# Kernel optimization log

Hardware: AMD Instinct MI355X
Metric: run time of the kernel (lower is better)

## Reference

```python
import jax, jax.numpy as jnp
import numpy as np

NUM_HEADS = 32
NUM_KV_HEADS = 8  # num_heads // 4 (GQA)
HEAD_DIM = 64     # hidden_size // num_heads
ROPE_BASE = 10000.0


def _rotate_half(x):
    x1, x2 = jnp.split(x, 2, axis=-1)
    return jnp.concatenate((-x2, x1), axis=-1)


def _rope_cos_sin(seq_len, dtype):
    inv_freq = 1.0 / (ROPE_BASE ** (jnp.arange(0, HEAD_DIM, 2, dtype=jnp.float32) / HEAD_DIM))
    t = jnp.arange(seq_len, dtype=jnp.float32)
    freqs = jnp.outer(t, inv_freq)                 # [S, HEAD_DIM//2]
    emb = jnp.concatenate((freqs, freqs), axis=-1) # [S, HEAD_DIM]
    return jnp.cos(emb).astype(dtype), jnp.sin(emb).astype(dtype)


def setup_inputs() -> dict:
    key = jax.random.key(0)
    ks = jax.random.split(key, 5)
    B, S, H = 1, 2048, 2048
    KV = NUM_KV_HEADS * HEAD_DIM  # 512
    s = 0.02
    return {
        "hidden_states": jax.random.normal(ks[0], (B, S, H), jnp.float32),
        "Wq": jax.random.normal(ks[1], (H, H), jnp.float32) * s,
        "Wk": jax.random.normal(ks[2], (KV, H), jnp.float32) * s,
        "Wv": jax.random.normal(ks[3], (KV, H), jnp.float32) * s,
        "Wo": jax.random.normal(ks[4], (H, H), jnp.float32) * s,
    }


def reference(hidden_states, Wq, Wk, Wv, Wo):
    B, S, H = hidden_states.shape
    dtype = hidden_states.dtype
    # QKV projections (nn.Linear with weight [out,in], no bias)
    q = jnp.einsum("bsh,oh->bso", hidden_states, Wq)
    k = jnp.einsum("bsh,oh->bso", hidden_states, Wk)
    v = jnp.einsum("bsh,oh->bso", hidden_states, Wv)
    q = q.reshape(B, S, NUM_HEADS, HEAD_DIM).transpose(0, 2, 1, 3)      # [B,H,S,D]
    k = k.reshape(B, S, NUM_KV_HEADS, HEAD_DIM).transpose(0, 2, 1, 3)   # [B,KV,S,D]
    v = v.reshape(B, S, NUM_KV_HEADS, HEAD_DIM).transpose(0, 2, 1, 3)
    # RoPE
    cos, sin = _rope_cos_sin(S, dtype)  # [S,D] broadcast over batch/heads
    q = q * cos + _rotate_half(q) * sin
    k = k * cos + _rotate_half(k) * sin
    # GQA: repeat_interleave KV heads
    groups = NUM_HEADS // NUM_KV_HEADS
    k = jnp.repeat(k, groups, axis=1)
    v = jnp.repeat(v, groups, axis=1)
    # Attention: scores in fp32 softmax, causal mask (additive)
    scale = 1.0 / np.sqrt(HEAD_DIM)
    scores = jnp.einsum("bhqd,bhkd->bhqk", q, k) * scale
    causal = jnp.tril(jnp.ones((S, S), dtype=bool))
    scores = jnp.where(causal, scores, jnp.finfo(jnp.float32).min)
    probs = jax.nn.softmax(scores.astype(jnp.float32), axis=-1).astype(dtype)
    attn = jnp.einsum("bhqk,bhkd->bhqd", probs, v)
    attn = attn.transpose(0, 2, 1, 3).reshape(B, S, H)
    return jnp.einsum("bsh,oh->bso", attn, Wo)
```

## Files before the change

### kernel.cpp

```cpp
#include <hip/hip_runtime.h>
#include <hip/hip_bf16.h>
#include <math.h>

typedef __hip_bfloat16 bf16;
typedef __attribute__((ext_vector_type(8))) short short8;
typedef __attribute__((ext_vector_type(4))) short short4v;
typedef __attribute__((ext_vector_type(4))) float floatx4;

#define MFMA16(a, b, c) __builtin_amdgcn_mfma_f32_16x16x32_bf16((a), (b), (c), 0, 0, 0)

typedef const __attribute__((address_space(1))) void* as1_cvp;
typedef __attribute__((address_space(3))) void* as3_vp;

__device__ __forceinline__ void gload_lds16(const bf16* g, bf16* lds_uni) {
    __builtin_amdgcn_global_load_lds((as1_cvp)g, (as3_vp)lds_uni, 16, 0, 0);
}

__global__ __launch_bounds__(256) void cvt_all(
    const float* __restrict__ a0, const float* __restrict__ a1,
    const float* __restrict__ a2, const float* __restrict__ a3,
    const float* __restrict__ a4,
    bf16* __restrict__ d0, bf16* __restrict__ d1, bf16* __restrict__ d2,
    bf16* __restrict__ d3, bf16* __restrict__ d4)
{
    const int b = blockIdx.x;
    const float* src; bf16* dst; int off;
    if (b < 2048)      { src = a0; dst = d0; off = b; }
    else if (b < 4096) { src = a1; dst = d1; off = b - 2048; }
    else if (b < 4608) { src = a2; dst = d2; off = b - 4096; }
    else if (b < 5120) { src = a3; dst = d3; off = b - 4608; }
    else               { src = a4; dst = d4; off = b - 5120; }
    const int i = (off * 256 + threadIdx.x) * 8;
    const float4 x = *(const float4*)(src + i);
    const float4 y = *(const float4*)(src + i + 4);
    bf16 t[8];
    t[0] = __float2bfloat16(x.x); t[1] = __float2bfloat16(x.y);
    t[2] = __float2bfloat16(x.z); t[3] = __float2bfloat16(x.w);
    t[4] = __float2bfloat16(y.x); t[5] = __float2bfloat16(y.y);
    t[6] = __float2bfloat16(y.z); t[7] = __float2bfloat16(y.w);
    *(short8*)(dst + i) = *(const short8*)t;
}

__global__ __launch_bounds__(256) void gemm_qkv(
    const bf16* __restrict__ A, const bf16* __restrict__ Wq,
    const bf16* __restrict__ Wk, const bf16* __restrict__ Wv,
    bf16* __restrict__ qb, bf16* __restrict__ kb, bf16* __restrict__ vt)
{
    constexpr int K = 2048;
    __shared__ bf16 As[128 * 32];
    __shared__ bf16 Bs[128 * 32];

    const int tid  = threadIdx.x;
    const int lane = tid & 63;
    const int w    = tid >> 6;
    const int wm   = w >> 1, wn = w & 1;
    const int quad = lane >> 4, l15 = lane & 15;
    const int bx = blockIdx.x, by = blockIdx.y;

    const bf16* Bp; int bxl, mode;
    if (bx < 16)      { Bp = Wq; bxl = bx;      mode = 0; }
    else if (bx < 20) { Bp = Wk; bxl = bx - 16; mode = 1; }
    else              { Bp = Wv; bxl = bx - 20; mode = 2; }

    floatx4 acc[4][4];
#pragma unroll
    for (int i = 0; i < 4; ++i)
#pragma unroll
        for (int j = 0; j < 4; ++j) {
            floatx4 z = {0.f, 0.f, 0.f, 0.f};
            acc[i][j] = z;
        }

    const int srow = tid >> 2;
    const int sch  = (tid & 3) * 8;
    const bf16* gA = A  + (size_t)(by * 128 + srow) * K + sch;
    const bf16* gB = Bp + (size_t)(bxl * 128 + srow) * K + sch;
    const size_t K64 = (size_t)64 * K;
    bf16* ldsA0 = As + w * 512;
    bf16* ldsA1 = As + 2048 + w * 512;
    bf16* ldsB0 = Bs + w * 512;
    bf16* ldsB1 = Bs + 2048 + w * 512;

    for (int k0 = 0; k0 < K; k0 += 32) {
        gload_lds16(gA + k0,        ldsA0);
        gload_lds16(gA + K64 + k0,  ldsA1);
        gload_lds16(gB + k0,        ldsB0);
        gload_lds16(gB + K64 + k0,  ldsB1);
        __syncthreads();

        short8 af[4], bfrag[4];
#pragma unroll
        for (int i = 0; i < 4; ++i)
            af[i] = *(const short8*)&As[(wm * 64 + i * 16 + l15) * 32 + quad * 8];
#pragma unroll
        for (int j = 0; j < 4; ++j)
            bfrag[j] = *(const short8*)&Bs[(wn * 64 + j * 16 + l15) * 32 + quad * 8];
#pragma unroll
        for (int i = 0; i < 4; ++i)
#pragma unroll
            for (int j = 0; j < 4; ++j)
                acc[i][j] = MFMA16(af[i], bfrag[j], acc[i][j]);
        __syncthreads();
    }

    if (mode == 2) {
#pragma unroll
        for (int i = 0; i < 4; ++i)
#pragma unroll
            for (int j = 0; j < 4; ++j) {
                const int col = bxl * 128 + wn * 64 + j * 16 + l15;
                const int rowb = by * 128 + wm * 64 + i * 16 + quad * 4;
                bf16 t[4];
#pragma unroll
                for (int r = 0; r < 4; ++r) t[r] = __float2bfloat16(acc[i][j][r]);
                *(short4v*)&vt[(size_t)col * 2048 + rowb] = *(const short4v*)t;
            }
    } else {
        const int Nn = (mode == 0) ? 2048 : 512;
        bf16* C = (mode == 0) ? qb : kb;
        const float scale = (mode == 0) ? 0.125f : 1.0f;
        const float LOG2_1E4 = 13.28771237954945f;
        const float ifr0 = exp2f(-((float)l15) * (LOG2_1E4 / 32.f));
        const float ifr1 = exp2f(-((float)(16 + l15)) * (LOG2_1E4 / 32.f));
#pragma unroll
        for (int i = 0; i < 4; ++i) {
#pragma unroll
            for (int r = 0; r < 4; ++r) {
                const int row = by * 128 + wm * 64 + i * 16 + quad * 4 + r;
                float s0, c0, s1, c1;
                sincosf((float)row * ifr0, &s0, &c0);
                sincosf((float)row * ifr1, &s1, &c1);
#pragma unroll
                for (int j = 0; j < 4; ++j) {
                    const float x  = acc[i][j][r];
                    const float xp = acc[i][j ^ 2][r];
                    const float cs = (j & 1) ? c1 : c0;
                    const float sn = (j & 1) ? s1 : s0;
                    const float oo = (x * cs + ((j < 2) ? -xp : xp) * sn) * scale;
                    const int col = bxl * 128 + wn * 64 + j * 16 + l15;
                    C[(size_t)row * Nn + col] = __float2bfloat16(oo);
                }
            }
        }
    }
}

__global__ __launch_bounds__(256) void gemm_out(
    const bf16* __restrict__ A, const bf16* __restrict__ B, float* __restrict__ C,
    int N, int K)
{
    __shared__ bf16 As[128 * 32];
    __shared__ bf16 Bs[128 * 32];

    const int tid  = threadIdx.x;
    const int lane = tid & 63;
    const int w    = tid >> 6;
    const int wm   = w >> 1, wn = w & 1;
    const int quad = lane >> 4, l15 = lane & 15;
    const int bx = blockIdx.x, by = blockIdx.y;

    floatx4 acc[4][4];
#pragma unroll
    for (int i = 0; i < 4; ++i)
#pragma unroll
        for (int j = 0; j < 4; ++j) {
            floatx4 z = {0.f, 0.f, 0.f, 0.f};
            acc[i][j] = z;
        }

    const int srow = tid >> 2;
    const int sch  = (tid & 3) * 8;
    const bf16* gA = A + (size_t)(by * 128 + srow) * K + sch;
    const bf16* gB = B + (size_t)(bx * 128 + srow) * K + sch;
    const size_t K64 = (size_t)64 * K;
    bf16* ldsA0 = As + w * 512;
    bf16* ldsA1 = As + 2048 + w * 512;
    bf16* ldsB0 = Bs + w * 512;
    bf16* ldsB1 = Bs + 2048 + w * 512;

    for (int k0 = 0; k0 < K; k0 += 32) {
        gload_lds16(gA + k0,        ldsA0);
        gload_lds16(gA + K64 + k0,  ldsA1);
        gload_lds16(gB + k0,        ldsB0);
        gload_lds16(gB + K64 + k0,  ldsB1);
        __syncthreads();

        short8 af[4], bfrag[4];
#pragma unroll
        for (int i = 0; i < 4; ++i)
            af[i] = *(const short8*)&As[(wm * 64 + i * 16 + l15) * 32 + quad * 8];
#pragma unroll
        for (int j = 0; j < 4; ++j)
            bfrag[j] = *(const short8*)&Bs[(wn * 64 + j * 16 + l15) * 32 + quad * 8];
#pragma unroll
        for (int i = 0; i < 4; ++i)
#pragma unroll
            for (int j = 0; j < 4; ++j)
                acc[i][j] = MFMA16(af[i], bfrag[j], acc[i][j]);
        __syncthreads();
    }

#pragma unroll
    for (int i = 0; i < 4; ++i)
#pragma unroll
        for (int j = 0; j < 4; ++j)
#pragma unroll
            for (int r = 0; r < 4; ++r) {
                const int row = by * 128 + wm * 64 + i * 16 + quad * 4 + r;
                const int col = bx * 128 + wn * 64 + j * 16 + l15;
                C[(size_t)row * N + col] = acc[i][j][r];
            }
}

__global__ __launch_bounds__(256) void fattn4(
    const bf16* __restrict__ q, const bf16* __restrict__ k,
    const bf16* __restrict__ vt, bf16* __restrict__ o)
{
    __shared__ bf16 Ks[2][64 * 72];
    __shared__ bf16 Vs[2][64 * 72];
    __shared__ bf16 Ps[4][16 * 68];

    const int tpair = blockIdx.x;
    const int h = blockIdx.y;
    const int kvh = h >> 2;
    const int tid = threadIdx.x, lane = tid & 63, w = tid >> 6;
    const int quad = lane >> 4, l15 = lane & 15;
    bf16* P = Ps[w];

    short ob[8];
#pragma unroll
    for (int e = 0; e < 8; ++e) ob[e] = (short)0x3F80;
    const short8 ones = *(const short8*)ob;

    const int srow = tid >> 3;
    const int ch8  = (tid & 7) * 8;
    const bf16* kg = k  + (size_t)kvh * 64 + ch8;
    const bf16* vg = vt + (size_t)(kvh * 64 + srow) * 2048 + ch8;

#pragma unroll 1
    for (int ph = 0; ph < 2; ++ph) {
        const int a = ph ? (31 - tpair) : tpair;
        const int qrow0 = a * 64 + w * 16;

        short8 qf[2];
#pragma unroll
        for (int ks = 0; ks < 2; ++ks)
            qf[ks] = *(const short8*)&q[(size_t)(qrow0 + l15) * 2048 + h * 64 + ks * 32 + quad * 8];

        floatx4 o_acc[4], l_acc;
#pragma unroll
        for (int n4 = 0; n4 < 4; ++n4) {
            floatx4 z = {0.f, 0.f, 0.f, 0.f};
            o_acc[n4] = z;
        }
        { floatx4 z = {0.f, 0.f, 0.f, 0.f}; l_acc = z; }

        {
            short8 k0 = *(const short8*)(kg + (size_t)srow * 512);
            short8 k1 = *(const short8*)(kg + (size_t)(srow + 32) * 512);
            short8 v0 = *(const short8*)(vg);
            short8 v1 = *(const short8*)(vg + (size_t)32 * 2048);
            *(short8*)&Ks[0][srow * 72 + ch8]        = k0;
            *(short8*)&Ks[0][(srow + 32) * 72 + ch8] = k1;
            *(short8*)&Vs[0][srow * 72 + ch8]        = v0;
            *(short8*)&Vs[0][(srow + 32) * 72 + ch8] = v1;
        }
        __syncthreads();

        for (int kt = 0; kt <= a; ++kt) {
            const int buf = kt & 1;

            short8 nk0, nk1, nv0, nv1;
            if (kt < a) {
                const size_t kr = (size_t)((kt + 1) * 64) * 512;
                nk0 = *(const short8*)(kg + kr + (size_t)srow * 512);
                nk1 = *(const short8*)(kg + kr + (size_t)(srow + 32) * 512);
                nv0 = *(const short8*)(vg + (kt + 1) * 64);
                nv1 = *(const short8*)(vg + (size_t)32 * 2048 + (kt + 1) * 64);
            }

            floatx4 s_acc[4];
#pragma unroll
            for (int n = 0; n < 4; ++n) {
                floatx4 z = {0.f, 0.f, 0.f, 0.f};
                s_acc[n] = z;
            }
#pragma unroll
            for (int n = 0; n < 4; ++n)
#pragma unroll
                for (int ks = 0; ks < 2; ++ks) {
                    const short8 kf = *(const short8*)&Ks[buf][(n * 16 + l15) * 72 + ks * 32 + quad * 8];
                    s_acc[n] = MFMA16(qf[ks], kf, s_acc[n]);
                }

            if (kt < a) {
#pragma unroll
                for (int n = 0; n < 4; ++n)
#pragma unroll
                    for (int r = 0; r < 4; ++r)
                        P[(quad * 4 + r) * 68 + n * 16 + l15] = __float2bfloat16(__expf(s_acc[n][r]));
            } else {
#pragma unroll
                for (int n = 0; n < 4; ++n)
#pragma unroll
                    for (int r = 0; r < 4; ++r) {
                        const bool ok = (n * 16 + l15) <= (w * 16 + quad * 4 + r);
                        const float p = ok ? __expf(s_acc[n][r]) : 0.f;
                        P[(quad * 4 + r) * 68 + n * 16 + l15] = __float2bfloat16(p);
                    }
            }

#pragma unroll
            for (int ks2 = 0; ks2 < 2; ++ks2) {
                const short8 pf = *(const short8*)&P[l15 * 68 + ks2 * 32 + quad * 8];
                l_acc = MFMA16(pf, ones, l_acc);
#pragma unroll
                for (int n4 = 0; n4 < 4; ++n4) {
                    const short8 vf = *(const short8*)&Vs[buf][(n4 * 16 + l15) * 72 + ks2 * 32 + quad * 8];
                    o_acc[n4] = MFMA16(pf, vf, o_acc[n4]);
                }
            }

            if (kt < a) {
                *(short8*)&Ks[buf ^ 1][srow * 72 + ch8]        = nk0;
                *(short8*)&Ks[buf ^ 1][(srow + 32) * 72 + ch8] = nk1;
                *(short8*)&Vs[buf ^ 1][srow * 72 + ch8]        = nv0;
                *(short8*)&Vs[buf ^ 1][(srow + 32) * 72 + ch8] = nv1;
            }
            __syncthreads();
        }

#pragma unroll
        for (int n4 = 0; n4 < 4; ++n4)
#pragma unroll
            for (int r = 0; r < 4; ++r) {
                const float val = o_acc[n4][r] / l_acc[r];
                const int row = qrow0 + quad * 4 + r;
                const int col = h * 64 + n4 * 16 + l15;
                o[(size_t)row * 2048 + col] = __float2bfloat16(val);
            }
    }
}

extern "C" void kernel_launch(void* const* d_in, const int* in_sizes, int n_in,
                              void* d_out, int out_size, void* d_ws, size_t ws_size,
                              hipStream_t stream)
{
    const float* hs = (const float*)d_in[0];
    const float* Wq = (const float*)d_in[1];
    const float* Wk = (const float*)d_in[2];
    const float* Wv = (const float*)d_in[3];
    const float* Wo = (const float*)d_in[4];
    float* out = (float*)d_out;

    bf16* ws  = (bf16*)d_ws;
    bf16* hsb = ws;
    bf16* Wqb = hsb + 4194304;
    bf16* Wkb = Wqb + 4194304;
    bf16* Wvb = Wkb + 1048576;
    bf16* Wob = Wvb + 1048576;
    bf16* qb  = Wob + 4194304;
    bf16* kb  = qb  + 4194304;
    bf16* vtb = kb  + 1048576;
    bf16* ab  = vtb + 1048576;

    dim3 blk(256);
    cvt_all<<<7168, blk, 0, stream>>>(hs, Wq, Wk, Wv, Wo, hsb, Wqb, Wkb, Wvb, Wob);
    gemm_qkv<<<dim3(24, 16), blk, 0, stream>>>(hsb, Wqb, Wkb, Wvb, qb, kb, vtb);
    fattn4<<<dim3(16, 32), blk, 0, stream>>>(qb, kb, vtb, ab);
    gemm_out<<<dim3(16, 16), blk, 0, stream>>>(ab, Wob, out, 2048, 2048);
}
```

Measured before the change: 248.9 us.

## Use 128x64 GEMM tiles with K=64 steps and transpose attention score MFMA

Both projection GEMMs now use 128x64 block tiles with four warps each owning 32 rows, and load 64 K-elements per barrier pair. This doubles the grid size so more CUs are occupied, and halves the number of sync iterations. In exchange, each block reuses the A tile across fewer output columns. The attention kernel swaps the MFMA operands for QK^T so each lane holds four consecutive keys, which allows vectorized 4-element P stores into LDS instead of scalar stores.

```diff
diff --git a/kernel.cpp b/kernel.cpp
--- a/kernel.cpp
+++ b/kernel.cpp
@@ -41,30 +41,56 @@
     *(short8*)(dst + i) = *(const short8*)t;
 }
 
+#define GEMM_K_LOOP_12864(KB)                                                   \
+    for (int k0 = 0; k0 < (KB); k0 += 64) {                                     \
+        gload_lds16(gA + k0,            ldsA);                                  \
+        gload_lds16(gA + A64 + k0,      ldsA + 2048);                           \
+        gload_lds16(gB + k0,            ldsB);                                  \
+        gload_lds16(gA + k0 + 32,       ldsA + 4096);                           \
+        gload_lds16(gA + A64 + k0 + 32, ldsA + 6144);                           \
+        gload_lds16(gB + k0 + 32,       ldsB + 2048);                           \
+        __syncthreads();                                                        \
+        _Pragma("unroll")                                                       \
+        for (int hh = 0; hh < 2; ++hh) {                                        \
+            short8 af[2], bfr[4];                                               \
+            _Pragma("unroll")                                                   \
+            for (int i = 0; i < 2; ++i)                                         \
+                af[i] = *(const short8*)&As[hh * 4096 + (w * 32 + i * 16 + l15) * 32 + quad * 8]; \
+            _Pragma("unroll")                                                   \
+            for (int j = 0; j < 4; ++j)                                         \
+                bfr[j] = *(const short8*)&Bs[hh * 2048 + (j * 16 + l15) * 32 + quad * 8]; \
+            _Pragma("unroll")                                                   \
+            for (int i = 0; i < 2; ++i)                                         \
+                _Pragma("unroll")                                               \
+                for (int j = 0; j < 4; ++j)                                     \
+                    acc[i][j] = MFMA16(af[i], bfr[j], acc[i][j]);               \
+        }                                                                       \
+        __syncthreads();                                                        \
+    }
+
 __global__ __launch_bounds__(256) void gemm_qkv(
     const bf16* __restrict__ A, const bf16* __restrict__ Wq,
     const bf16* __restrict__ Wk, const bf16* __restrict__ Wv,
     bf16* __restrict__ qb, bf16* __restrict__ kb, bf16* __restrict__ vt)
 {
-    constexpr int K = 2048;
-    __shared__ bf16 As[128 * 32];
-    __shared__ bf16 Bs[128 * 32];
+    constexpr int LDK = 2048;
+    __shared__ bf16 As[2 * 128 * 32];
+    __shared__ bf16 Bs[2 * 64 * 32];
 
     const int tid  = threadIdx.x;
     const int lane = tid & 63;
     const int w    = tid >> 6;
-    const int wm   = w >> 1, wn = w & 1;
     const int quad = lane >> 4, l15 = lane & 15;
     const int bx = blockIdx.x, by = blockIdx.y;
 
     const bf16* Bp; int bxl, mode;
-    if (bx < 16)      { Bp = Wq; bxl = bx;      mode = 0; }
-    else if (bx < 20) { Bp = Wk; bxl = bx - 16; mode = 1; }
-    else              { Bp = Wv; bxl = bx - 20; mode = 2; }
-
-    floatx4 acc[4][4];
-#pragma unroll
-    for (int i = 0; i < 4; ++i)
+    if (bx < 32)      { Bp = Wq; bxl = bx;      mode = 0; }
+    else if (bx < 40) { Bp = Wk; bxl = bx - 32; mode = 1; }
+    else              { Bp = Wv; bxl = bx - 40; mode = 2; }
+
+    floatx4 acc[2][4];
+#pragma unroll
+    for (int i = 0; i < 2; ++i)
 #pragma unroll
         for (int j = 0; j < 4; ++j) {
             floatx4 z = {0.f, 0.f, 0.f, 0.f};
@@ -73,60 +99,38 @@
 
     const int srow = tid >> 2;
     const int sch  = (tid & 3) * 8;
-    const bf16* gA = A  + (size_t)(by * 128 + srow) * K + sch;
-    const bf16* gB = Bp + (size_t)(bxl * 128 + srow) * K + sch;
-    const size_t K64 = (size_t)64 * K;
-    bf16* ldsA0 = As + w * 512;
-    bf16* ldsA1 = As + 2048 + w * 512;
-    bf16* ldsB0 = Bs + w * 512;
-    bf16* ldsB1 = Bs + 2048 + w * 512;
-
-    for (int k0 = 0; k0 < K; k0 += 32) {
-        gload_lds16(gA + k0,        ldsA0);
-        gload_lds16(gA + K64 + k0,  ldsA1);
-        gload_lds16(gB + k0,        ldsB0);
-        gload_lds16(gB + K64 + k0,  ldsB1);
-        __syncthreads();
-
-        short8 af[4], bfrag[4];
-#pragma unroll
-        for (int i = 0; i < 4; ++i)
-            af[i] = *(const short8*)&As[(wm * 64 + i * 16 + l15) * 32 + quad * 8];
-#pragma unroll
-        for (int j = 0; j < 4; ++j)
-            bfrag[j] = *(const short8*)&Bs[(wn * 64 + j * 16 + l15) * 32 + quad * 8];
-#pragma unroll
-        for (int i = 0; i < 4; ++i)
-#pragma unroll
-            for (int j = 0; j < 4; ++j)
-                acc[i][j] = MFMA16(af[i], bfrag[j], acc[i][j]);
-        __syncthreads();
-    }
+    const bf16* gA = A  + (size_t)(by * 128 + srow) * LDK + sch;
+    const bf16* gB = Bp + (size_t)(bxl * 64 + srow) * LDK + sch;
+    const size_t A64 = (size_t)64 * LDK;
+    bf16* ldsA = As + w * 512;
+    bf16* ldsB = Bs + w * 512;
+
+    GEMM_K_LOOP_12864(LDK)
 
     if (mode == 2) {
 #pragma unroll
-        for (int i = 0; i < 4; ++i)
+        for (int i = 0; i < 2; ++i)
 #pragma unroll
             for (int j = 0; j < 4; ++j) {
-                const int col = bxl * 128 + wn * 64 + j * 16 + l15;
-                const int rowb = by * 128 + wm * 64 + i * 16 + quad * 4;
+                const int col = bxl * 64 + j * 16 + l15;
+                const int rowb = by * 128 + w * 32 + i * 16 + quad * 4;
                 bf16 t[4];
 #pragma unroll
                 for (int r = 0; r < 4; ++r) t[r] = __float2bfloat16(acc[i][j][r]);
                 *(short4v*)&vt[(size_t)col * 2048 + rowb] = *(const short4v*)t;
             }
     } else {
+        bf16* C = (mode == 0) ? qb : kb;
         const int Nn = (mode == 0) ? 2048 : 512;
-        bf16* C = (mode == 0) ? qb : kb;
         const float scale = (mode == 0) ? 0.125f : 1.0f;
         const float LOG2_1E4 = 13.28771237954945f;
         const float ifr0 = exp2f(-((float)l15) * (LOG2_1E4 / 32.f));
         const float ifr1 = exp2f(-((float)(16 + l15)) * (LOG2_1E4 / 32.f));
 #pragma unroll
-        for (int i = 0; i < 4; ++i) {
+        for (int i = 0; i < 2; ++i) {
 #pragma unroll
             for (int r = 0; r < 4; ++r) {
-                const int row = by * 128 + wm * 64 + i * 16 + quad * 4 + r;
+                const int row = by * 128 + w * 32 + i * 16 + quad * 4 + r;
                 float s0, c0, s1, c1;
                 sincosf((float)row * ifr0, &s0, &c0);
                 sincosf((float)row * ifr1, &s1, &c1);
@@ -137,7 +141,7 @@
                     const float cs = (j & 1) ? c1 : c0;
                     const float sn = (j & 1) ? s1 : s0;
                     const float oo = (x * cs + ((j < 2) ? -xp : xp) * sn) * scale;
-                    const int col = bxl * 128 + wn * 64 + j * 16 + l15;
+                    const int col = bxl * 64 + j * 16 + l15;
                     C[(size_t)row * Nn + col] = __float2bfloat16(oo);
                 }
             }
@@ -146,22 +150,21 @@
 }
 
 __global__ __launch_bounds__(256) void gemm_out(
-    const bf16* __restrict__ A, const bf16* __restrict__ B, float* __restrict__ C,
-    int N, int K)
-{
-    __shared__ bf16 As[128 * 32];
-    __shared__ bf16 Bs[128 * 32];
+    const bf16* __restrict__ A, const bf16* __restrict__ B, float* __restrict__ C)
+{
+    constexpr int LDK = 2048;
+    __shared__ bf16 As[2 * 128 * 32];
+    __shared__ bf16 Bs[2 * 64 * 32];
 
     const int tid  = threadIdx.x;
     const int lane = tid & 63;
     const int w    = tid >> 6;
-    const int wm   = w >> 1, wn = w & 1;
     const int quad = lane >> 4, l15 = lane & 15;
     const int bx = blockIdx.x, by = blockIdx.y;
 
-    floatx4 acc[4][4];
-#pragma unroll
-    for (int i = 0; i < 4; ++i)
+    floatx4 acc[2][4];
+#pragma unroll
+    for (int i = 0; i < 2; ++i)
 #pragma unroll
         for (int j = 0; j < 4; ++j) {
             floatx4 z = {0.f, 0.f, 0.f, 0.f};
@@ -170,49 +173,27 @@
 
     const int srow = tid >> 2;
     const int sch  = (tid & 3) * 8;
-    const bf16* gA = A + (size_t)(by * 128 + srow) * K + sch;
-    const bf16* gB = B + (size_t)(bx * 128 + srow) * K + sch;
-    const size_t K64 = (size_t)64 * K;
-    bf16* ldsA0 = As + w * 512;
-    bf16* ldsA1 = As + 2048 + w * 512;
-    bf16* ldsB0 = Bs + w * 512;
-    bf16* ldsB1 = Bs + 2048 + w * 512;
-
-    for (int k0 = 0; k0 < K; k0 += 32) {
-        gload_lds16(gA + k0,        ldsA0);
-        gload_lds16(gA + K64 + k0,  ldsA1);
-        gload_lds16(gB + k0,        ldsB0);
-        gload_lds16(gB + K64 + k0,  ldsB1);
-        __syncthreads();
-
-        short8 af[4], bfrag[4];
-#pragma unroll
-        for (int i = 0; i < 4; ++i)
-            af[i] = *(const short8*)&As[(wm * 64 + i * 16 + l15) * 32 + quad * 8];
+    const bf16* gA = A + (size_t)(by * 128 + srow) * LDK + sch;
+    const bf16* gB = B + (size_t)(bx * 64 + srow) * LDK + sch;
+    const size_t A64 = (size_t)64 * LDK;
+    bf16* ldsA = As + w * 512;
+    bf16* ldsB = Bs + w * 512;
+
+    GEMM_K_LOOP_12864(LDK)
+
+#pragma unroll
+    for (int i = 0; i < 2; ++i)
 #pragma unroll
         for (int j = 0; j < 4; ++j)
-            bfrag[j] = *(const short8*)&Bs[(wn * 64 + j * 16 + l15) * 32 + quad * 8];
-#pragma unroll
-        for (int i = 0; i < 4; ++i)
-#pragma unroll
-            for (int j = 0; j < 4; ++j)
-                acc[i][j] = MFMA16(af[i], bfrag[j], acc[i][j]);
-        __syncthreads();
-    }
-
-#pragma unroll
-    for (int i = 0; i < 4; ++i)
-#pragma unroll
-        for (int j = 0; j < 4; ++j)
 #pragma unroll
             for (int r = 0; r < 4; ++r) {
-                const int row = by * 128 + wm * 64 + i * 16 + quad * 4 + r;
-                const int col = bx * 128 + wn * 64 + j * 16 + l15;
-                C[(size_t)row * N + col] = acc[i][j][r];
-            }
-}
-
-__global__ __launch_bounds__(256) void fattn4(
+                const int row = by * 128 + w * 32 + i * 16 + quad * 4 + r;
+                const int col = bx * 64 + j * 16 + l15;
+                C[(size_t)row * 2048 + col] = acc[i][j][r];
+            }
+}
+
+__global__ __launch_bounds__(256) void fattn4b(
     const bf16* __restrict__ q, const bf16* __restrict__ k,
     const bf16* __restrict__ vt, bf16* __restrict__ o)
 {
@@ -290,24 +271,29 @@
 #pragma unroll
                 for (int ks = 0; ks < 2; ++ks) {
                     const short8 kf = *(const short8*)&Ks[buf][(n * 16 + l15) * 72 + ks * 32 + quad * 8];
-                    s_acc[n] = MFMA16(qf[ks], kf, s_acc[n]);
+                    s_acc[n] = MFMA16(kf, qf[ks], s_acc[n]);
                 }
 
             if (kt < a) {
 #pragma unroll
-                for (int n = 0; n < 4; ++n)
+                for (int n = 0; n < 4; ++n) {
+                    bf16 t4[4];
 #pragma unroll
                     for (int r = 0; r < 4; ++r)
-                        P[(quad * 4 + r) * 68 + n * 16 + l15] = __float2bfloat16(__expf(s_acc[n][r]));
+                        t4[r] = __float2bfloat16(__expf(s_acc[n][r]));
+                    *(short4v*)&P[l15 * 68 + n * 16 + quad * 4] = *(const short4v*)t4;
+                }
             } else {
 #pragma unroll
-                for (int n = 0; n < 4; ++n)
+                for (int n = 0; n < 4; ++n) {
+                    bf16 t4[4];
 #pragma unroll
                     for (int r = 0; r < 4; ++r) {
-                        const bool ok = (n * 16 + l15) <= (w * 16 + quad * 4 + r);
-                        const float p = ok ? __expf(s_acc[n][r]) : 0.f;
-                        P[(quad * 4 + r) * 68 + n * 16 + l15] = __float2bfloat16(p);
+                        const bool okc = (n * 16 + quad * 4 + r) <= (w * 16 + l15);
+                        t4[r] = __float2bfloat16(okc ? __expf(s_acc[n][r]) : 0.f);
                     }
+                    *(short4v*)&P[l15 * 68 + n * 16 + quad * 4] = *(const short4v*)t4;
+                }
             }
 
 #pragma unroll
@@ -355,18 +341,18 @@
 
     bf16* ws  = (bf16*)d_ws;
     bf16* hsb = ws;
-    bf16* Wqb = hsb + 4194304;
-    bf16* Wkb = Wqb + 4194304;
-    bf16* Wvb = Wkb + 1048576;
-    bf16* Wob = Wvb + 1048576;
-    bf16* qb  = Wob + 4194304;
-    bf16* kb  = qb  + 4194304;
-    bf16* vtb = kb  + 1048576;
-    bf16* ab  = vtb + 1048576;
+    bf16* Wqb = ws + 4194304;
+    bf16* Wkb = ws + 8388608;
+    bf16* Wvb = ws + 9437184;
+    bf16* Wob = ws + 10485760;
+    bf16* qb  = ws + 14680064;
+    bf16* kb  = ws + 18874368;
+    bf16* vtb = ws + 19922944;
+    bf16* ab  = ws + 20971520;
 
     dim3 blk(256);
     cvt_all<<<7168, blk, 0, stream>>>(hs, Wq, Wk, Wv, Wo, hsb, Wqb, Wkb, Wvb, Wob);
-    gemm_qkv<<<dim3(24, 16), blk, 0, stream>>>(hsb, Wqb, Wkb, Wvb, qb, kb, vtb);
-    fattn4<<<dim3(16, 32), blk, 0, stream>>>(qb, kb, vtb, ab);
-    gemm_out<<<dim3(16, 16), blk, 0, stream>>>(ab, Wob, out, 2048, 2048);
-}
+    gemm_qkv<<<dim3(48, 16), blk, 0, stream>>>(hsb, Wqb, Wkb, Wvb, qb, kb, vtb);
+    fattn4b<<<dim3(16, 32), blk, 0, stream>>>(qb, kb, vtb, ab);
+    gemm_out<<<dim3(32, 16), blk, 0, stream>>>(ab, Wob, out);
+}
```

After: 223.0 us. -10.4%, faster.
